# Kernel tuning notes

Hardware: AMD Instinct MI355X
Metric: run time of the kernel (lower is better)

The kernel has to match this reference:

```python
import jax, jax.numpy as jnp
import numpy as np

HEIGHT = 32
NEG = -1e30
K = 2
DEPTH_LIM = 3
BN_EPS = 1e-5


def blockwise_knn(x, k, depth_lim):
    # x: [B, C, N]. Returns global neighbor indices [B, N, k*width].
    B, C, N = x.shape
    width = N // HEIGHT
    k_eff = k * width
    xb = x.reshape(B, C, HEIGHT, width)
    win = 2 * depth_lim + 1
    offs = jnp.arange(win) - depth_lim

    def per_block(i):
        wb = i + offs
        valid = (wb >= 0) & (wb < HEIGHT)
        wbc = jnp.clip(wb, 0, HEIGHT - 1)
        cand = xb[:, :, wbc, :].reshape(B, C, win * width)   # [B,C,W]
        q = xb[:, :, i, :]                                   # [B,C,width]
        # negative squared distance: 2 q.c - |q|^2 - |c|^2 (topk largest = nearest)
        d = 2.0 * jnp.einsum('bcq,bcw->bqw', q, cand)
        d = d - jnp.sum(q * q, axis=1)[:, :, None] - jnp.sum(cand * cand, axis=1)[:, None, :]
        mask = jnp.repeat(valid, width)                      # [W]
        d = jnp.where(mask[None, None, :], d, NEG)
        _, loc = jax.lax.top_k(d, k_eff)                     # [B,width,k_eff]
        # window starts at block (i-depth_lim): local -> global point index
        return loc + (i - depth_lim) * width

    idx = jax.vmap(per_block, out_axes=1)(jnp.arange(HEIGHT))  # [B,32,width,k_eff]
    return idx.reshape(B, N, k_eff)


def get_graph_feature(x, k, depth_lim):
    B, C, N = x.shape
    idx = blockwise_knn(x, k, depth_lim)              # [B,N,K] int32
    xt = jnp.transpose(x, (0, 2, 1))                  # [B,N,C]
    feat = jax.vmap(lambda xb, ib: xb[ib])(xt, idx)   # [B,N,K,C] gather
    center = xt[:, :, None, :]
    f = jnp.concatenate([feat - center, jnp.broadcast_to(center, feat.shape)], axis=-1)
    return jnp.transpose(f, (0, 3, 1, 2))             # [B,2C,N,K]


def edge_layer(x, w, g, b, k, depth_lim):
    f = get_graph_feature(x, k, depth_lim)            # [B,2C,N,K]
    y = jnp.einsum('oc,bcnk->bonk', w, f)             # 1x1 conv, no bias
    # BatchNorm2d, train-mode batch statistics (biased variance)
    mu = jnp.mean(y, axis=(0, 2, 3), keepdims=True)
    var = jnp.mean((y - mu) ** 2, axis=(0, 2, 3), keepdims=True)
    y = (y - mu) / jnp.sqrt(var + BN_EPS) * g[None, :, None, None] + b[None, :, None, None]
    y = jnp.where(y >= 0, y, 0.2 * y)                 # LeakyReLU(0.2)
    return jnp.max(y, axis=-1)                        # max over neighbors -> [B,O,N]


def setup_inputs() -> dict:
    key = jax.random.key(0)
    ks = jax.random.split(key, 16)
    d = {}
    d['x'] = jax.random.normal(ks[0], (2, 256, 1024), jnp.float32)
    shapes = {'w0': (128, 512), 'w1': (128, 256), 'w2': (64, 256), 'w3': (64, 128)}
    for i, (name, sh) in enumerate(shapes.items()):
        d[name] = jax.random.normal(ks[1 + i], sh, jnp.float32) * (1.0 / np.sqrt(sh[1]))
        co = sh[0]
        d['g' + name[1]] = jax.random.uniform(ks[5 + i], (co,), jnp.float32, 0.5, 1.5)
        d['b' + name[1]] = jax.random.normal(ks[9 + i], (co,), jnp.float32) * 0.1
    d['w_last'] = jax.random.normal(ks[13], (384, 384), jnp.float32) * (1.0 / np.sqrt(384))
    return d


def reference(x, w0, g0, b0, w1, g1, b1, w2, g2, b2, w3, g3, b3, w_last):
    x0 = edge_layer(x, w0, g0, b0, K, DEPTH_LIM)          # [B,128,N]
    xnew = edge_layer(x0, w1, g1, b1, K, DEPTH_LIM)       # [B,128,N]
    xcon = jnp.concatenate([x0, xnew], axis=1)            # [B,256,N]
    xnew = edge_layer(xnew, w2, g2, b2, K, DEPTH_LIM)     # [B,64,N]
    xcon = jnp.concatenate([xcon, xnew], axis=1)          # [B,320,N]
    xnew = edge_layer(xnew, w3, g3, b3, K, DEPTH_LIM)     # [B,64,N]
    xcon = jnp.concatenate([xcon, xnew], axis=1)          # [B,384,N]
    return jnp.einsum('oc,bcn->bon', w_last, xcon)        # Conv1d k=1, no bias
```

## Files before the change

kernel.cpp:

```cpp
#include <hip/hip_runtime.h>
#include <math.h>

#define NPTS 1024
#define CAND 224
#define KEFF 64
#define BATCH 2
#define NEGV -1e30f

__global__ __launch_bounds__(256) void kprep(const float* __restrict__ w0, const float* __restrict__ w1,
                                             const float* __restrict__ w2, const float* __restrict__ w3,
                                             const float* __restrict__ wl, float* __restrict__ wt) {
    __shared__ float tA[32][33];
    __shared__ float tB[32][33];
    int id = blockIdx.x;
    int t = threadIdx.x;
    int row = t >> 5, col = t & 31;
    const float* W = w0; int Cin = 256, Co = 128; float* WtA = wt; float* WtB = wt + 32768;
    int tc = 0, to = 0; bool isWL = false;
    if (id < 32)      { int r = id;      tc = r >> 2; to = r & 3; }
    else if (id < 48) { W = w1; Cin = 128; Co = 128; WtA = wt + 65536;  WtB = wt + 81920;  int r = id - 32; tc = r >> 2; to = r & 3; }
    else if (id < 56) { W = w2; Cin = 128; Co = 64;  WtA = wt + 98304;  WtB = wt + 106496; int r = id - 48; tc = r >> 1; to = r & 1; }
    else if (id < 60) { W = w3; Cin = 64;  Co = 64;  WtA = wt + 114688; WtB = wt + 118784; int r = id - 56; tc = r >> 1; to = r & 1; }
    else { isWL = true; int r = id - 60; tc = r / 12; to = r % 12; }
    if (!isWL) {
#pragma unroll
        for (int r = 0; r < 4; ++r) {
            int o = to * 32 + row + r * 8;
            int c = tc * 32 + col;
            float va = W[(size_t)o * 2 * Cin + c];
            tA[row + r * 8][col] = va;
            tB[row + r * 8][col] = W[(size_t)o * 2 * Cin + Cin + c] - va;
        }
        __syncthreads();
#pragma unroll
        for (int r = 0; r < 4; ++r) {
            int c = tc * 32 + row + r * 8;
            int o = to * 32 + col;
            WtA[(size_t)c * Co + o] = tA[col][row + r * 8];
            WtB[(size_t)c * Co + o] = tB[col][row + r * 8];
        }
    } else {
        float* wlT = wt + 122880;
#pragma unroll
        for (int r = 0; r < 4; ++r) {
            int o = to * 32 + row + r * 8;
            int c = tc * 32 + col;
            tA[row + r * 8][col] = wl[(size_t)o * 384 + c];
        }
        __syncthreads();
#pragma unroll
        for (int r = 0; r < 4; ++r) {
            int c = tc * 32 + row + r * 8;
            int o = to * 32 + col;
            wlT[(size_t)c * 384 + o] = tA[col][row + r * 8];
        }
    }
}

struct GP {
    const float* xin; int bstride; int Cin; int Co; int nch; int applyBN;
    const float* WtA; const float* WtB;
    const float* partPrev; const float* gPrev; const float* bePrev;
    float* A; float* Bv; float* sq; float* Dp;
};

__global__ __launch_bounds__(256) void kgemm(GP p) {
    __shared__ float smem[7168];
    __shared__ float shsc[128];
    __shared__ float shsh[128];
    int t = threadIdx.x;
    if (p.applyBN && t < p.Cin) {
        const float* pp = p.partPrev;
        float s  = pp[t * 2]     + pp[(p.Cin + t) * 2];
        float s2 = pp[t * 2 + 1] + pp[(p.Cin + t) * 2 + 1];
        const float invc = 1.f / 131072.f;
        float mu = s * invc;
        float var = s2 * invc - mu * mu;
        float rs = rsqrtf(var + 1e-5f);
        float sc = p.gPrev[t] * rs;
        shsc[t] = sc;
        shsh[t] = p.bePrev[t] - mu * sc;
    }
    __syncthreads();
    int nABx = 16 * (p.Co >> 6) * BATCH;
    if ((int)blockIdx.x < nABx) {
        int id = blockIdx.x;
        int nt = id & 15; int rest = id >> 4;
        int nOT = p.Co >> 6;
        int ot = rest % nOT; int b = rest / nOT;
        int tn4 = (t & 15) * 4, to4 = (t >> 4) * 4;
        int n0 = nt * 64, o0 = ot * 64;
        const float* xb = p.xin + (size_t)b * p.bstride + n0;
        float* Xs = smem; float* Wta = smem + 2048; float* Wtb = smem + 4224;
        float4 a[4], bb[4], s4;
#pragma unroll
        for (int i = 0; i < 4; ++i) { a[i] = make_float4(0.f,0.f,0.f,0.f); bb[i] = make_float4(0.f,0.f,0.f,0.f); }
        s4 = make_float4(0.f,0.f,0.f,0.f);
        int cc0 = t >> 6, nn0 = t & 63;
        for (int c0 = 0; c0 < p.Cin; c0 += 32) {
            float rx[8], ra[8], rb[8];
#pragma unroll
            for (int k = 0; k < 8; ++k) {
                int cc = cc0 + k * 4;
                rx[k] = xb[(size_t)(c0 + cc) * NPTS + nn0];
                ra[k] = p.WtA[(size_t)(c0 + cc) * p.Co + o0 + nn0];
                rb[k] = p.WtB[(size_t)(c0 + cc) * p.Co + o0 + nn0];
            }
            if (p.applyBN) {
#pragma unroll
                for (int k = 0; k < 8; ++k) {
                    int cc = cc0 + k * 4;
                    float y = fmaf(rx[k], shsc[c0 + cc], shsh[c0 + cc]);
                    rx[k] = y >= 0.f ? y : 0.2f * y;
                }
            }
            __syncthreads();
#pragma unroll
            for (int k = 0; k < 8; ++k) {
                int cc = cc0 + k * 4;
                Xs[cc * 64 + nn0] = rx[k];
                Wta[cc * 68 + nn0] = ra[k];
                Wtb[cc * 68 + nn0] = rb[k];
            }
            __syncthreads();
#pragma unroll 4
            for (int cc = 0; cc < 32; ++cc) {
                float4 xv = *(const float4*)&Xs[cc * 64 + tn4];
                float4 wa = *(const float4*)&Wta[cc * 68 + to4];
                float4 wb = *(const float4*)&Wtb[cc * 68 + to4];
                s4.x = fmaf(xv.x, xv.x, s4.x);
                s4.y = fmaf(xv.y, xv.y, s4.y);
                s4.z = fmaf(xv.z, xv.z, s4.z);
                s4.w = fmaf(xv.w, xv.w, s4.w);
                float wav[4] = {wa.x, wa.y, wa.z, wa.w};
                float wbv[4] = {wb.x, wb.y, wb.z, wb.w};
#pragma unroll
                for (int i = 0; i < 4; ++i) {
                    a[i].x  = fmaf(wav[i], xv.x, a[i].x);
                    a[i].y  = fmaf(wav[i], xv.y, a[i].y);
                    a[i].z  = fmaf(wav[i], xv.z, a[i].z);
                    a[i].w  = fmaf(wav[i], xv.w, a[i].w);
                    bb[i].x = fmaf(wbv[i], xv.x, bb[i].x);
                    bb[i].y = fmaf(wbv[i], xv.y, bb[i].y);
                    bb[i].z = fmaf(wbv[i], xv.z, bb[i].z);
                    bb[i].w = fmaf(wbv[i], xv.w, bb[i].w);
                }
            }
        }
        int n = n0 + tn4;
        if (ot == 0 && to4 == 0)
            *(float4*)&p.sq[b * NPTS + n] = s4;
#pragma unroll
        for (int i = 0; i < 4; ++i) {
            int o = o0 + to4 + i;
            size_t off = ((size_t)(b * p.Co + o)) * NPTS + n;
            *(float4*)&p.A[off] = a[i];
            *(float4*)&p.Bv[off] = bb[i];
        }
    } else {
        int id2 = blockIdx.x - nABx;
        int chunk = id2 % p.nch; int rest = id2 / p.nch;
        int i = rest & 31; int b = rest >> 5;
        const float* xb = p.xin + (size_t)b * p.bstride;
        float* Xc = smem;
        int q = t >> 3;
        int wg = t & 7;
        float acc[28];
#pragma unroll
        for (int j = 0; j < 28; ++j) acc[j] = 0.f;
        for (int sub = 0; sub < 2; ++sub) {
            int c0 = chunk * 64 + sub * 32;
            if (c0 >= p.Cin) break;
            float r[28];
            int rcc[28], rw[28];
#pragma unroll
            for (int k = 0; k < 28; ++k) {
                int e = t + k * 256;
                int cc = e / CAND;
                int w  = e - cc * CAND;
                rcc[k] = cc; rw[k] = w;
                int wb = i - 3 + (w >> 5);
                wb = wb < 0 ? 0 : (wb > 31 ? 31 : wb);
                r[k] = xb[(size_t)(c0 + cc) * NPTS + wb * 32 + (w & 31)];
            }
            if (p.applyBN) {
#pragma unroll
                for (int k = 0; k < 28; ++k) {
                    float y = fmaf(r[k], shsc[c0 + rcc[k]], shsh[c0 + rcc[k]]);
                    r[k] = y >= 0.f ? y : 0.2f * y;
                }
            }
            __syncthreads();
#pragma unroll
            for (int k = 0; k < 28; ++k)
                Xc[rcc[k] * CAND + rw[k]] = r[k];
            __syncthreads();
            for (int cc = 0; cc < 32; ++cc) {
                float qv = Xc[cc * CAND + 96 + q];
                const float4* row = (const float4*)&Xc[cc * CAND + wg * 28];
#pragma unroll
                for (int j4 = 0; j4 < 7; ++j4) {
                    float4 v = row[j4];
                    acc[j4 * 4 + 0] = fmaf(qv, v.x, acc[j4 * 4 + 0]);
                    acc[j4 * 4 + 1] = fmaf(qv, v.y, acc[j4 * 4 + 1]);
                    acc[j4 * 4 + 2] = fmaf(qv, v.z, acc[j4 * 4 + 2]);
                    acc[j4 * 4 + 3] = fmaf(qv, v.w, acc[j4 * 4 + 3]);
                }
            }
        }
        int n = i * 32 + q;
        size_t base = (((size_t)chunk * BATCH + b) * NPTS + n) * CAND + wg * 28;
        float4* outp = (float4*)&p.Dp[base];
#pragma unroll
        for (int j4 = 0; j4 < 7; ++j4)
            outp[j4] = make_float4(acc[j4 * 4], acc[j4 * 4 + 1], acc[j4 * 4 + 2], acc[j4 * 4 + 3]);
    }
}

template<int NCH>
__global__ __launch_bounds__(256) void kselect(const float* __restrict__ Dp,
                                               const float* __restrict__ sq,
                                               int* __restrict__ idxo) {
    __shared__ ulonglong2 Dsh2[4][112];
    unsigned long long* Dsh = (unsigned long long*)Dsh2;
    int t = threadIdx.x;
    int wv = t >> 6, l = t & 63;
    int b = blockIdx.y;
    int n = blockIdx.x * 4 + wv;
    int i = n >> 5;
    float sqn = sq[b * NPTS + n];
    float pr[4][NCH];
    float sqw[4];
#pragma unroll
    for (int j = 0; j < 4; ++j) {
        int w = l + 64 * j;
        if (w < CAND) {
            size_t off = ((size_t)b * NPTS + n) * CAND + w;
#pragma unroll
            for (int ch = 0; ch < NCH; ++ch)
                pr[j][ch] = Dp[off + (size_t)ch * (BATCH * NPTS * CAND)];
            int wb = i - 3 + (w >> 5);
            int wbc = wb < 0 ? 0 : (wb > 31 ? 31 : wb);
            sqw[j] = sq[b * NPTS + wbc * 32 + (w & 31)];
        }
    }
    unsigned long long kj[4];
#pragma unroll
    for (int j = 0; j < 4; ++j) {
        int w = l + 64 * j;
        if (w < CAND) {
            float s = 0.f;
#pragma unroll
            for (int ch = 0; ch < NCH; ++ch) s += pr[j][ch];
            int wb = i - 3 + (w >> 5);
            bool valid = (wb >= 0) && (wb < 32);
            float d = 2.f * s - sqn - sqw[j];
            d = valid ? d : NEGV;
            unsigned u = __float_as_uint(d);
            u ^= ((unsigned)((int)u >> 31)) | 0x80000000u;
            unsigned long long key = ((unsigned long long)u << 8) | (unsigned long long)(255 - w);
            kj[j] = key;
            Dsh[wv * 224 + w] = key;
        } else {
            kj[j] = 0ull;
        }
    }
    __syncthreads();
    int cnt[4] = {0, 0, 0, 0};
    const ulonglong2* row = Dsh2[wv];
#pragma unroll 2
    for (int w2 = 0; w2 < 112; w2 += 4) {
        ulonglong2 k0 = row[w2], k1 = row[w2 + 1], k2 = row[w2 + 2], k3 = row[w2 + 3];
#pragma unroll
        for (int j = 0; j < 4; ++j) {
            unsigned long long kk = kj[j];
            cnt[j] += (int)(k0.x > kk) + (int)(k0.y > kk) + (int)(k1.x > kk) + (int)(k1.y > kk)
                    + (int)(k2.x > kk) + (int)(k2.y > kk) + (int)(k3.x > kk) + (int)(k3.y > kk);
        }
    }
#pragma unroll
    for (int j = 0; j < 4; ++j) {
        int w = l + 64 * j;
        if (w < CAND && cnt[j] < KEFF)
            idxo[((size_t)b * NPTS + n) * KEFF + cnt[j]] = (i - 3) * 32 + w;
    }
}

__global__ __launch_bounds__(256) void kagg(const float* __restrict__ A, const float* __restrict__ Bv,
                                            const int* __restrict__ idx, int Co,
                                            float* __restrict__ xconM, int chOut,
                                            float* __restrict__ part) {
    __shared__ float Ash[NPTS];
    __shared__ float red[256];
    int o = blockIdx.x, b = blockIdx.y, t = threadIdx.x;
    size_t rowoff = ((size_t)(b * Co + o)) * NPTS;
    {
        float rA[4];
#pragma unroll
        for (int r = 0; r < 4; ++r) rA[r] = A[rowoff + r * 256 + t];
#pragma unroll
        for (int r = 0; r < 4; ++r) Ash[r * 256 + t] = rA[r];
    }
    __syncthreads();
    float sum = 0.f, sumsq = 0.f;
    for (int r = 0; r < 4; ++r) {
        int n = r * 256 + t;
        const int4* ip = (const int4*)&idx[((size_t)b * NPTS + n) * KEFF];
        float s1 = 0.f, s2 = 0.f, mx = -3.4e38f;
#pragma unroll
        for (int kk = 0; kk < KEFF / 4; ++kk) {
            int4 v4 = ip[kk];
            float a0 = Ash[v4.x], a1 = Ash[v4.y], a2 = Ash[v4.z], a3 = Ash[v4.w];
            s1 += a0 + a1 + a2 + a3;
            s2 += a0 * a0 + a1 * a1 + a2 * a2 + a3 * a3;
            mx = fmaxf(mx, fmaxf(fmaxf(a0, a1), fmaxf(a2, a3)));
        }
        float bv = Bv[rowoff + n];
        xconM[((size_t)b * 384 + chOut + o) * NPTS + n] = mx + bv;
        sum   += s1 + 64.f * bv;
        sumsq += s2 + 2.f * bv * s1 + 64.f * bv * bv;
    }
    red[t] = sum; __syncthreads();
    for (int s = 128; s > 0; s >>= 1) { if (t < s) red[t] += red[t + s]; __syncthreads(); }
    if (t == 0) part[((size_t)(b * Co + o)) * 2 + 0] = red[0];
    __syncthreads();
    red[t] = sumsq; __syncthreads();
    for (int s = 128; s > 0; s >>= 1) { if (t < s) red[t] += red[t + s]; __syncthreads(); }
    if (t == 0) part[((size_t)(b * Co + o)) * 2 + 1] = red[0];
}

struct FP {
    const float* part0; const float* part1; const float* part2; const float* part3;
    const float* g0; const float* g1; const float* g2; const float* g3;
    const float* be0; const float* be1; const float* be2; const float* be3;
};

__global__ __launch_bounds__(256) void kfinal(const float* __restrict__ xconM,
                                              const float* __restrict__ wlT, FP p,
                                              float* __restrict__ out) {
    __shared__ float Xs[2048];
    __shared__ float Wl[2176];
    __shared__ float shsc[384];
    __shared__ float shsh[384];
    int t = threadIdx.x;
    for (int ch = t; ch < 384; ch += 256) {
        const float* pl; const float* gl; const float* bl; int o, Col;
        if (ch < 128)      { pl = p.part0; gl = p.g0; bl = p.be0; o = ch;       Col = 128; }
        else if (ch < 256) { pl = p.part1; gl = p.g1; bl = p.be1; o = ch - 128; Col = 128; }
        else if (ch < 320) { pl = p.part2; gl = p.g2; bl = p.be2; o = ch - 256; Col = 64;  }
        else               { pl = p.part3; gl = p.g3; bl = p.be3; o = ch - 320; Col = 64;  }
        float s  = pl[o * 2]     + pl[(Col + o) * 2];
        float s2 = pl[o * 2 + 1] + pl[(Col + o) * 2 + 1];
        const float invc = 1.f / 131072.f;
        float mu = s * invc;
        float var = s2 * invc - mu * mu;
        float rs = rsqrtf(var + 1e-5f);
        float sc = gl[o] * rs;
        shsc[ch] = sc;
        shsh[ch] = bl[o] - mu * sc;
    }
    __syncthreads();
    int tn4 = (t & 15) * 4, to4 = (t >> 4) * 4;
    int n0 = blockIdx.x * 64, o0 = blockIdx.y * 64, b = blockIdx.z;
    int cc0 = t >> 6, nn0 = t & 63;
    float4 acc[4];
#pragma unroll
    for (int i = 0; i < 4; ++i) acc[i] = make_float4(0.f,0.f,0.f,0.f);
    for (int c0 = 0; c0 < 384; c0 += 32) {
        float rx[8], rw[8];
#pragma unroll
        for (int k = 0; k < 8; ++k) {
            int cc = cc0 + k * 4;
            rx[k] = xconM[((size_t)b * 384 + c0 + cc) * NPTS + n0 + nn0];
            rw[k] = wlT[(size_t)(c0 + cc) * 384 + o0 + nn0];
        }
#pragma unroll
        for (int k = 0; k < 8; ++k) {
            int cc = cc0 + k * 4;
            float y = fmaf(rx[k], shsc[c0 + cc], shsh[c0 + cc]);
            rx[k] = y >= 0.f ? y : 0.2f * y;
        }
        __syncthreads();
#pragma unroll
        for (int k = 0; k < 8; ++k) {
            int cc = cc0 + k * 4;
            Xs[cc * 64 + nn0] = rx[k];
            Wl[cc * 68 + nn0] = rw[k];
        }
        __syncthreads();
#pragma unroll 4
        for (int cc = 0; cc < 32; ++cc) {
            float4 xv = *(const float4*)&Xs[cc * 64 + tn4];
            float4 wv = *(const float4*)&Wl[cc * 68 + to4];
            float wvv[4] = {wv.x, wv.y, wv.z, wv.w};
#pragma unroll
            for (int i = 0; i < 4; ++i) {
                acc[i].x = fmaf(wvv[i], xv.x, acc[i].x);
                acc[i].y = fmaf(wvv[i], xv.y, acc[i].y);
                acc[i].z = fmaf(wvv[i], xv.z, acc[i].z);
                acc[i].w = fmaf(wvv[i], xv.w, acc[i].w);
            }
        }
    }
#pragma unroll
    for (int i = 0; i < 4; ++i)
        *(float4*)&out[((size_t)b * 384 + o0 + to4 + i) * NPTS + n0 + tn4] = acc[i];
}

extern "C" void kernel_launch(void* const* d_in, const int* in_sizes, int n_in,
                              void* d_out, int out_size, void* d_ws, size_t ws_size,
                              hipStream_t stream) {
    const float* x  = (const float*)d_in[0];
    const float* w[4]  = {(const float*)d_in[1], (const float*)d_in[4], (const float*)d_in[7], (const float*)d_in[10]};
    const float* g[4]  = {(const float*)d_in[2], (const float*)d_in[5], (const float*)d_in[8], (const float*)d_in[11]};
    const float* be[4] = {(const float*)d_in[3], (const float*)d_in[6], (const float*)d_in[9], (const float*)d_in[12]};
    const float* wl = (const float*)d_in[13];

    float* ws    = (float*)d_ws;
    float* xconM = ws;
    float* A     = xconM + 786432;
    float* Bv    = A + 262144;
    float* sq    = Bv + 262144;
    float* Dp    = sq + 2048;
    float* part  = Dp + 1835008;
    float* wt    = part + 2048;
    int*   idx   = (int*)(wt + 270336);

    kprep<<<204, 256, 0, stream>>>(w[0], w[1], w[2], w[3], wl, wt);

    struct LC { const float* xin; int bstride; int Cin; int Co; int nch; int chOut;
                const float* wtA; const float* wtB; };
    LC L[4] = {
        { x,                  256 * 1024, 256, 128, 4, 0,   wt,          wt + 32768  },
        { xconM,              384 * 1024, 128, 128, 2, 128, wt + 65536,  wt + 81920  },
        { xconM + 128 * 1024, 384 * 1024, 128, 64,  2, 256, wt + 98304,  wt + 106496 },
        { xconM + 256 * 1024, 384 * 1024, 64,  64,  1, 320, wt + 114688, wt + 118784 },
    };

    for (int l = 0; l < 4; ++l) {
        GP gp;
        gp.xin = L[l].xin; gp.bstride = L[l].bstride; gp.Cin = L[l].Cin; gp.Co = L[l].Co;
        gp.nch = L[l].nch; gp.applyBN = (l > 0);
        gp.WtA = L[l].wtA; gp.WtB = L[l].wtB;
        gp.partPrev = (l > 0) ? part + (l - 1) * 512 : nullptr;
        gp.gPrev = (l > 0) ? g[l - 1] : nullptr;
        gp.bePrev = (l > 0) ? be[l - 1] : nullptr;
        gp.A = A; gp.Bv = Bv; gp.sq = sq; gp.Dp = Dp;
        int nAB = 16 * (L[l].Co >> 6) * BATCH;
        int nDist = L[l].nch * 32 * BATCH;
        kgemm  <<<nAB + nDist, 256, 0, stream>>>(gp);
        if (L[l].nch == 4)      kselect<4><<<dim3(NPTS / 4, BATCH), 256, 0, stream>>>(Dp, sq, idx);
        else if (L[l].nch == 2) kselect<2><<<dim3(NPTS / 4, BATCH), 256, 0, stream>>>(Dp, sq, idx);
        else                    kselect<1><<<dim3(NPTS / 4, BATCH), 256, 0, stream>>>(Dp, sq, idx);
        kagg   <<<dim3(L[l].Co, BATCH), 256, 0, stream>>>(A, Bv, idx, L[l].Co, xconM, L[l].chOut, part + l * 512);
    }

    FP fp;
    fp.part0 = part; fp.part1 = part + 512; fp.part2 = part + 1024; fp.part3 = part + 1536;
    fp.g0 = g[0]; fp.g1 = g[1]; fp.g2 = g[2]; fp.g3 = g[3];
    fp.be0 = be[0]; fp.be1 = be[1]; fp.be2 = be[2]; fp.be3 = be[3];
    kfinal<<<dim3(16, 6, BATCH), 256, 0, stream>>>(xconM, wt + 122880, fp, (float*)d_out);
}
```

Measured before the change: 277.1 us.

## Fuse distance computation and top-k selection into the GEMM kernel

Merges the kselect kernel into the distance blocks of the GEMM kernel. Each block now loops over all channel chunks itself, computes the squared norms of the candidate window locally, and ranks the 224 candidate keys in shared memory. This removes the Dp partial-distance buffer, the global sq array and one launch per layer. In exchange only 64 distance blocks run per layer, down from up to 256 chunk-split blocks, and each thread holds 28 keys and 28 counters, which raises register pressure and lowers parallelism.

New measurement: 411.8 us. 1.49x slower.

```diff
diff --git a/kernel.cpp b/kernel.cpp
--- a/kernel.cpp
+++ b/kernel.cpp
@@ -58,16 +58,18 @@
 }
 
 struct GP {
-    const float* xin; int bstride; int Cin; int Co; int nch; int applyBN;
+    const float* xin; int bstride; int Cin; int Co; int applyBN;
     const float* WtA; const float* WtB;
     const float* partPrev; const float* gPrev; const float* bePrev;
-    float* A; float* Bv; float* sq; float* Dp;
+    float* A; float* Bv; int* idxo;
 };
 
-__global__ __launch_bounds__(256) void kgemm(GP p) {
-    __shared__ float smem[7168];
+__global__ __launch_bounds__(256) void kfused(GP p) {
+    __shared__ __align__(16) unsigned long long sKeys[32 * 224];
+    __shared__ float sqc[224];
     __shared__ float shsc[128];
     __shared__ float shsh[128];
+    float* smem = (float*)sKeys;
     int t = threadIdx.x;
     if (p.applyBN && t < p.Cin) {
         const float* pp = p.partPrev;
@@ -92,10 +94,9 @@
         int n0 = nt * 64, o0 = ot * 64;
         const float* xb = p.xin + (size_t)b * p.bstride + n0;
         float* Xs = smem; float* Wta = smem + 2048; float* Wtb = smem + 4224;
-        float4 a[4], bb[4], s4;
+        float4 a[4], bb[4];
 #pragma unroll
         for (int i = 0; i < 4; ++i) { a[i] = make_float4(0.f,0.f,0.f,0.f); bb[i] = make_float4(0.f,0.f,0.f,0.f); }
-        s4 = make_float4(0.f,0.f,0.f,0.f);
         int cc0 = t >> 6, nn0 = t & 63;
         for (int c0 = 0; c0 < p.Cin; c0 += 32) {
             float rx[8], ra[8], rb[8];
@@ -128,10 +129,6 @@
                 float4 xv = *(const float4*)&Xs[cc * 64 + tn4];
                 float4 wa = *(const float4*)&Wta[cc * 68 + to4];
                 float4 wb = *(const float4*)&Wtb[cc * 68 + to4];
-                s4.x = fmaf(xv.x, xv.x, s4.x);
-                s4.y = fmaf(xv.y, xv.y, s4.y);
-                s4.z = fmaf(xv.z, xv.z, s4.z);
-                s4.w = fmaf(xv.w, xv.w, s4.w);
                 float wav[4] = {wa.x, wa.y, wa.z, wa.w};
                 float wbv[4] = {wb.x, wb.y, wb.z, wb.w};
 #pragma unroll
@@ -148,8 +145,6 @@
             }
         }
         int n = n0 + tn4;
-        if (ot == 0 && to4 == 0)
-            *(float4*)&p.sq[b * NPTS + n] = s4;
 #pragma unroll
         for (int i = 0; i < 4; ++i) {
             int o = o0 + to4 + i;
@@ -159,130 +154,109 @@
         }
     } else {
         int id2 = blockIdx.x - nABx;
-        int chunk = id2 % p.nch; int rest = id2 / p.nch;
-        int i = rest & 31; int b = rest >> 5;
+        int i = id2 & 31, b = id2 >> 5;
         const float* xb = p.xin + (size_t)b * p.bstride;
         float* Xc = smem;
         int q = t >> 3;
         int wg = t & 7;
-        float acc[28];
-#pragma unroll
-        for (int j = 0; j < 28; ++j) acc[j] = 0.f;
-        for (int sub = 0; sub < 2; ++sub) {
-            int c0 = chunk * 64 + sub * 32;
-            if (c0 >= p.Cin) break;
-            float r[28];
-            int rcc[28], rw[28];
-#pragma unroll
-            for (int k = 0; k < 28; ++k) {
-                int e = t + k * 256;
-                int cc = e / CAND;
-                int w  = e - cc * CAND;
-                rcc[k] = cc; rw[k] = w;
-                int wb = i - 3 + (w >> 5);
-                wb = wb < 0 ? 0 : (wb > 31 ? 31 : wb);
-                r[k] = xb[(size_t)(c0 + cc) * NPTS + wb * 32 + (w & 31)];
-            }
-            if (p.applyBN) {
+        float s28[28];
+#pragma unroll
+        for (int j = 0; j < 28; ++j) s28[j] = 0.f;
+        float sqacc = 0.f;
+        int nch = (p.Cin + 63) >> 6;
+        for (int chunk = 0; chunk < nch; ++chunk) {
+            float cacc[28];
+#pragma unroll
+            for (int j = 0; j < 28; ++j) cacc[j] = 0.f;
+            for (int sub = 0; sub < 2; ++sub) {
+                int c0 = chunk * 64 + sub * 32;
+                if (c0 >= p.Cin) break;
+                float r[28];
+                int rcc[28], rw[28];
 #pragma unroll
                 for (int k = 0; k < 28; ++k) {
-                    float y = fmaf(r[k], shsc[c0 + rcc[k]], shsh[c0 + rcc[k]]);
-                    r[k] = y >= 0.f ? y : 0.2f * y;
-                }
-            }
-            __syncthreads();
-#pragma unroll
-            for (int k = 0; k < 28; ++k)
-                Xc[rcc[k] * CAND + rw[k]] = r[k];
-            __syncthreads();
-            for (int cc = 0; cc < 32; ++cc) {
-                float qv = Xc[cc * CAND + 96 + q];
-                const float4* row = (const float4*)&Xc[cc * CAND + wg * 28];
-#pragma unroll
-                for (int j4 = 0; j4 < 7; ++j4) {
-                    float4 v = row[j4];
-                    acc[j4 * 4 + 0] = fmaf(qv, v.x, acc[j4 * 4 + 0]);
-                    acc[j4 * 4 + 1] = fmaf(qv, v.y, acc[j4 * 4 + 1]);
-                    acc[j4 * 4 + 2] = fmaf(qv, v.z, acc[j4 * 4 + 2]);
-                    acc[j4 * 4 + 3] = fmaf(qv, v.w, acc[j4 * 4 + 3]);
-                }
-            }
-        }
-        int n = i * 32 + q;
-        size_t base = (((size_t)chunk * BATCH + b) * NPTS + n) * CAND + wg * 28;
-        float4* outp = (float4*)&p.Dp[base];
-#pragma unroll
-        for (int j4 = 0; j4 < 7; ++j4)
-            outp[j4] = make_float4(acc[j4 * 4], acc[j4 * 4 + 1], acc[j4 * 4 + 2], acc[j4 * 4 + 3]);
-    }
-}
-
-template<int NCH>
-__global__ __launch_bounds__(256) void kselect(const float* __restrict__ Dp,
-                                               const float* __restrict__ sq,
-                                               int* __restrict__ idxo) {
-    __shared__ ulonglong2 Dsh2[4][112];
-    unsigned long long* Dsh = (unsigned long long*)Dsh2;
-    int t = threadIdx.x;
-    int wv = t >> 6, l = t & 63;
-    int b = blockIdx.y;
-    int n = blockIdx.x * 4 + wv;
-    int i = n >> 5;
-    float sqn = sq[b * NPTS + n];
-    float pr[4][NCH];
-    float sqw[4];
-#pragma unroll
-    for (int j = 0; j < 4; ++j) {
-        int w = l + 64 * j;
-        if (w < CAND) {
-            size_t off = ((size_t)b * NPTS + n) * CAND + w;
-#pragma unroll
-            for (int ch = 0; ch < NCH; ++ch)
-                pr[j][ch] = Dp[off + (size_t)ch * (BATCH * NPTS * CAND)];
-            int wb = i - 3 + (w >> 5);
-            int wbc = wb < 0 ? 0 : (wb > 31 ? 31 : wb);
-            sqw[j] = sq[b * NPTS + wbc * 32 + (w & 31)];
-        }
-    }
-    unsigned long long kj[4];
-#pragma unroll
-    for (int j = 0; j < 4; ++j) {
-        int w = l + 64 * j;
-        if (w < CAND) {
-            float s = 0.f;
-#pragma unroll
-            for (int ch = 0; ch < NCH; ++ch) s += pr[j][ch];
+                    int e = t + k * 256;
+                    int cc = e / CAND;
+                    int w  = e - cc * CAND;
+                    rcc[k] = cc; rw[k] = w;
+                    int wb = i - 3 + (w >> 5);
+                    wb = wb < 0 ? 0 : (wb > 31 ? 31 : wb);
+                    r[k] = xb[(size_t)(c0 + cc) * NPTS + wb * 32 + (w & 31)];
+                }
+                if (p.applyBN) {
+#pragma unroll
+                    for (int k = 0; k < 28; ++k) {
+                        float y = fmaf(r[k], shsc[c0 + rcc[k]], shsh[c0 + rcc[k]]);
+                        r[k] = y >= 0.f ? y : 0.2f * y;
+                    }
+                }
+                __syncthreads();
+#pragma unroll
+                for (int k = 0; k < 28; ++k)
+                    Xc[rcc[k] * CAND + rw[k]] = r[k];
+                __syncthreads();
+                if (t < CAND) {
+#pragma unroll 8
+                    for (int cc = 0; cc < 32; ++cc) {
+                        float v = Xc[cc * CAND + t];
+                        sqacc = fmaf(v, v, sqacc);
+                    }
+                }
+                for (int cc = 0; cc < 32; ++cc) {
+                    float qv = Xc[cc * CAND + 96 + q];
+                    const float4* row = (const float4*)&Xc[cc * CAND + wg * 28];
+#pragma unroll
+                    for (int j4 = 0; j4 < 7; ++j4) {
+                        float4 v = row[j4];
+                        cacc[j4 * 4 + 0] = fmaf(qv, v.x, cacc[j4 * 4 + 0]);
+                        cacc[j4 * 4 + 1] = fmaf(qv, v.y, cacc[j4 * 4 + 1]);
+                        cacc[j4 * 4 + 2] = fmaf(qv, v.z, cacc[j4 * 4 + 2]);
+                        cacc[j4 * 4 + 3] = fmaf(qv, v.w, cacc[j4 * 4 + 3]);
+                    }
+                }
+            }
+#pragma unroll
+            for (int j = 0; j < 28; ++j) s28[j] += cacc[j];
+        }
+        if (t < CAND) sqc[t] = sqacc;
+        __syncthreads();
+        float sqn = sqc[96 + q];
+        unsigned long long kj[28];
+#pragma unroll
+        for (int j = 0; j < 28; ++j) {
+            int w = wg * 28 + j;
             int wb = i - 3 + (w >> 5);
             bool valid = (wb >= 0) && (wb < 32);
-            float d = 2.f * s - sqn - sqw[j];
+            float d = 2.f * s28[j] - sqn - sqc[w];
             d = valid ? d : NEGV;
             unsigned u = __float_as_uint(d);
             u ^= ((unsigned)((int)u >> 31)) | 0x80000000u;
-            unsigned long long key = ((unsigned long long)u << 8) | (unsigned long long)(255 - w);
-            kj[j] = key;
-            Dsh[wv * 224 + w] = key;
-        } else {
-            kj[j] = 0ull;
-        }
-    }
-    __syncthreads();
-    int cnt[4] = {0, 0, 0, 0};
-    const ulonglong2* row = Dsh2[wv];
-#pragma unroll 2
-    for (int w2 = 0; w2 < 112; w2 += 4) {
-        ulonglong2 k0 = row[w2], k1 = row[w2 + 1], k2 = row[w2 + 2], k3 = row[w2 + 3];
-#pragma unroll
-        for (int j = 0; j < 4; ++j) {
-            unsigned long long kk = kj[j];
-            cnt[j] += (int)(k0.x > kk) + (int)(k0.y > kk) + (int)(k1.x > kk) + (int)(k1.y > kk)
-                    + (int)(k2.x > kk) + (int)(k2.y > kk) + (int)(k3.x > kk) + (int)(k3.y > kk);
-        }
-    }
-#pragma unroll
-    for (int j = 0; j < 4; ++j) {
-        int w = l + 64 * j;
-        if (w < CAND && cnt[j] < KEFF)
-            idxo[((size_t)b * NPTS + n) * KEFF + cnt[j]] = (i - 3) * 32 + w;
+            kj[j] = ((unsigned long long)u << 8) | (unsigned long long)(255 - w);
+        }
+#pragma unroll
+        for (int j = 0; j < 28; ++j)
+            sKeys[q * 224 + wg * 28 + j] = kj[j];
+        __syncthreads();
+        int cnt[28];
+#pragma unroll
+        for (int j = 0; j < 28; ++j) cnt[j] = 0;
+        const ulonglong2* row = (const ulonglong2*)(sKeys + q * 224);
+        for (int c2 = 0; c2 < 112; c2 += 4) {
+            ulonglong2 k0 = row[c2], k1 = row[c2 + 1], k2 = row[c2 + 2], k3 = row[c2 + 3];
+#pragma unroll
+            for (int j = 0; j < 28; ++j) {
+                unsigned long long kk = kj[j];
+                cnt[j] += (int)(k0.x > kk) + (int)(k0.y > kk) + (int)(k1.x > kk) + (int)(k1.y > kk)
+                        + (int)(k2.x > kk) + (int)(k2.y > kk) + (int)(k3.x > kk) + (int)(k3.y > kk);
+            }
+        }
+        int n = i * 32 + q;
+#pragma unroll
+        for (int j = 0; j < 28; ++j) {
+            int w = wg * 28 + j;
+            if (cnt[j] < KEFF)
+                p.idxo[((size_t)b * NPTS + n) * KEFF + cnt[j]] = (i - 3) * 32 + w;
+        }
     }
 }
 
@@ -420,39 +394,33 @@
     float* xconM = ws;
     float* A     = xconM + 786432;
     float* Bv    = A + 262144;
-    float* sq    = Bv + 262144;
-    float* Dp    = sq + 2048;
-    float* part  = Dp + 1835008;
+    float* part  = Bv + 262144;
     float* wt    = part + 2048;
     int*   idx   = (int*)(wt + 270336);
 
     kprep<<<204, 256, 0, stream>>>(w[0], w[1], w[2], w[3], wl, wt);
 
-    struct LC { const float* xin; int bstride; int Cin; int Co; int nch; int chOut;
+    struct LC { const float* xin; int bstride; int Cin; int Co; int chOut;
                 const float* wtA; const float* wtB; };
     LC L[4] = {
-        { x,                  256 * 1024, 256, 128, 4, 0,   wt,          wt + 32768  },
-        { xconM,              384 * 1024, 128, 128, 2, 128, wt + 65536,  wt + 81920  },
-        { xconM + 128 * 1024, 384 * 1024, 128, 64,  2, 256, wt + 98304,  wt + 106496 },
-        { xconM + 256 * 1024, 384 * 1024, 64,  64,  1, 320, wt + 114688, wt + 118784 },
+        { x,                  256 * 1024, 256, 128, 0,   wt,          wt + 32768  },
+        { xconM,              384 * 1024, 128, 128, 128, wt + 65536,  wt + 81920  },
+        { xconM + 128 * 1024, 384 * 1024, 128, 64,  256, wt + 98304,  wt + 106496 },
+        { xconM + 256 * 1024, 384 * 1024, 64,  64,  320, wt + 114688, wt + 118784 },
     };
 
     for (int l = 0; l < 4; ++l) {
         GP gp;
         gp.xin = L[l].xin; gp.bstride = L[l].bstride; gp.Cin = L[l].Cin; gp.Co = L[l].Co;
-        gp.nch = L[l].nch; gp.applyBN = (l > 0);
+        gp.applyBN = (l > 0);
         gp.WtA = L[l].wtA; gp.WtB = L[l].wtB;
         gp.partPrev = (l > 0) ? part + (l - 1) * 512 : nullptr;
         gp.gPrev = (l > 0) ? g[l - 1] : nullptr;
         gp.bePrev = (l > 0) ? be[l - 1] : nullptr;
-        gp.A = A; gp.Bv = Bv; gp.sq = sq; gp.Dp = Dp;
+        gp.A = A; gp.Bv = Bv; gp.idxo = idx;
         int nAB = 16 * (L[l].Co >> 6) * BATCH;
-        int nDist = L[l].nch * 32 * BATCH;
-        kgemm  <<<nAB + nDist, 256, 0, stream>>>(gp);
-        if (L[l].nch == 4)      kselect<4><<<dim3(NPTS / 4, BATCH), 256, 0, stream>>>(Dp, sq, idx);
-        else if (L[l].nch == 2) kselect<2><<<dim3(NPTS / 4, BATCH), 256, 0, stream>>>(Dp, sq, idx);
-        else                    kselect<1><<<dim3(NPTS / 4, BATCH), 256, 0, stream>>>(Dp, sq, idx);
-        kagg   <<<dim3(L[l].Co, BATCH), 256, 0, stream>>>(A, Bv, idx, L[l].Co, xconM, L[l].chOut, part + l * 512);
+        kfused<<<nAB + 64, 256, 0, stream>>>(gp);
+        kagg  <<<dim3(L[l].Co, BATCH), 256, 0, stream>>>(A, Bv, idx, L[l].Co, xconM, L[l].chOut, part + l * 512);
     }
 
     FP fp;
```

## Split GEMM and distance work into more blocks, transpose neighbor index layout

Applied to the files above, without the earlier changes.

The A/B projection GEMM tiles shrink from 64 to 32 points, doubling the block count. The distance blocks now each handle a single 32-channel slice, which doubles the number of channel chunks and the partial-distance buffer that kselect must sum. The neighbor index array is stored k-major, so kagg threads read the indices for consecutive points with coalesced loads. The aim is more parallelism on a small problem, paid for with extra partial-sum memory traffic in kselect and a larger workspace.

Result: faster. 258.7 us, median of 2 (-6.7%).

```diff
diff --git a/kernel.cpp b/kernel.cpp
--- a/kernel.cpp
+++ b/kernel.cpp
@@ -6,6 +6,7 @@
 #define KEFF 64
 #define BATCH 2
 #define NEGV -1e30f
+#define PLANE (BATCH * NPTS * CAND)
 
 __global__ __launch_bounds__(256) void kprep(const float* __restrict__ w0, const float* __restrict__ w1,
                                              const float* __restrict__ w2, const float* __restrict__ w3,
@@ -82,130 +83,123 @@
         shsh[t] = p.bePrev[t] - mu * sc;
     }
     __syncthreads();
-    int nABx = 16 * (p.Co >> 6) * BATCH;
+    int nOT = p.Co >> 6;
+    int nABx = 32 * nOT * BATCH;
     if ((int)blockIdx.x < nABx) {
         int id = blockIdx.x;
-        int nt = id & 15; int rest = id >> 4;
-        int nOT = p.Co >> 6;
+        int nt = id & 31; int rest = id >> 5;
         int ot = rest % nOT; int b = rest / nOT;
-        int tn4 = (t & 15) * 4, to4 = (t >> 4) * 4;
-        int n0 = nt * 64, o0 = ot * 64;
+        int tn2 = (t & 15) * 2, to4 = (t >> 4) * 4;
+        int n0 = nt * 32, o0 = ot * 64;
         const float* xb = p.xin + (size_t)b * p.bstride + n0;
-        float* Xs = smem; float* Wta = smem + 2048; float* Wtb = smem + 4224;
-        float4 a[4], bb[4], s4;
-#pragma unroll
-        for (int i = 0; i < 4; ++i) { a[i] = make_float4(0.f,0.f,0.f,0.f); bb[i] = make_float4(0.f,0.f,0.f,0.f); }
-        s4 = make_float4(0.f,0.f,0.f,0.f);
-        int cc0 = t >> 6, nn0 = t & 63;
+        float* Xs = smem; float* Wta = smem + 1024; float* Wtb = smem + 3200;
+        float2 a2[4], b2[4], s2v;
+#pragma unroll
+        for (int i = 0; i < 4; ++i) { a2[i] = make_float2(0.f,0.f); b2[i] = make_float2(0.f,0.f); }
+        s2v = make_float2(0.f,0.f);
+        int xcc0 = t >> 5, xnn = t & 31;
+        int wcc0 = t >> 6, woo = t & 63;
         for (int c0 = 0; c0 < p.Cin; c0 += 32) {
-            float rx[8], ra[8], rb[8];
+            float rx[4], ra[8], rb[8];
+#pragma unroll
+            for (int k = 0; k < 4; ++k)
+                rx[k] = xb[(size_t)(c0 + xcc0 + k * 8) * NPTS + xnn];
 #pragma unroll
             for (int k = 0; k < 8; ++k) {
-                int cc = cc0 + k * 4;
-                rx[k] = xb[(size_t)(c0 + cc) * NPTS + nn0];
-                ra[k] = p.WtA[(size_t)(c0 + cc) * p.Co + o0 + nn0];
-                rb[k] = p.WtB[(size_t)(c0 + cc) * p.Co + o0 + nn0];
+                ra[k] = p.WtA[(size_t)(c0 + wcc0 + k * 4) * p.Co + o0 + woo];
+                rb[k] = p.WtB[(size_t)(c0 + wcc0 + k * 4) * p.Co + o0 + woo];
             }
             if (p.applyBN) {
 #pragma unroll
-                for (int k = 0; k < 8; ++k) {
-                    int cc = cc0 + k * 4;
+                for (int k = 0; k < 4; ++k) {
+                    int cc = xcc0 + k * 8;
                     float y = fmaf(rx[k], shsc[c0 + cc], shsh[c0 + cc]);
                     rx[k] = y >= 0.f ? y : 0.2f * y;
                 }
             }
             __syncthreads();
 #pragma unroll
+            for (int k = 0; k < 4; ++k)
+                Xs[(xcc0 + k * 8) * 32 + xnn] = rx[k];
+#pragma unroll
             for (int k = 0; k < 8; ++k) {
-                int cc = cc0 + k * 4;
-                Xs[cc * 64 + nn0] = rx[k];
-                Wta[cc * 68 + nn0] = ra[k];
-                Wtb[cc * 68 + nn0] = rb[k];
+                Wta[(wcc0 + k * 4) * 68 + woo] = ra[k];
+                Wtb[(wcc0 + k * 4) * 68 + woo] = rb[k];
             }
             __syncthreads();
-#pragma unroll 4
+#pragma unroll 8
             for (int cc = 0; cc < 32; ++cc) {
-                float4 xv = *(const float4*)&Xs[cc * 64 + tn4];
+                float2 xv = *(const float2*)&Xs[cc * 32 + tn2];
                 float4 wa = *(const float4*)&Wta[cc * 68 + to4];
                 float4 wb = *(const float4*)&Wtb[cc * 68 + to4];
-                s4.x = fmaf(xv.x, xv.x, s4.x);
-                s4.y = fmaf(xv.y, xv.y, s4.y);
-                s4.z = fmaf(xv.z, xv.z, s4.z);
-                s4.w = fmaf(xv.w, xv.w, s4.w);
+                s2v.x = fmaf(xv.x, xv.x, s2v.x);
+                s2v.y = fmaf(xv.y, xv.y, s2v.y);
                 float wav[4] = {wa.x, wa.y, wa.z, wa.w};
                 float wbv[4] = {wb.x, wb.y, wb.z, wb.w};
 #pragma unroll
                 for (int i = 0; i < 4; ++i) {
-                    a[i].x  = fmaf(wav[i], xv.x, a[i].x);
-                    a[i].y  = fmaf(wav[i], xv.y, a[i].y);
-                    a[i].z  = fmaf(wav[i], xv.z, a[i].z);
-                    a[i].w  = fmaf(wav[i], xv.w, a[i].w);
-                    bb[i].x = fmaf(wbv[i], xv.x, bb[i].x);
-                    bb[i].y = fmaf(wbv[i], xv.y, bb[i].y);
-                    bb[i].z = fmaf(wbv[i], xv.z, bb[i].z);
-                    bb[i].w = fmaf(wbv[i], xv.w, bb[i].w);
+                    a2[i].x = fmaf(wav[i], xv.x, a2[i].x);
+                    a2[i].y = fmaf(wav[i], xv.y, a2[i].y);
+                    b2[i].x = fmaf(wbv[i], xv.x, b2[i].x);
+                    b2[i].y = fmaf(wbv[i], xv.y, b2[i].y);
                 }
             }
         }
-        int n = n0 + tn4;
+        int n = n0 + tn2;
         if (ot == 0 && to4 == 0)
-            *(float4*)&p.sq[b * NPTS + n] = s4;
+            *(float2*)&p.sq[b * NPTS + n] = s2v;
 #pragma unroll
         for (int i = 0; i < 4; ++i) {
             int o = o0 + to4 + i;
             size_t off = ((size_t)(b * p.Co + o)) * NPTS + n;
-            *(float4*)&p.A[off] = a[i];
-            *(float4*)&p.Bv[off] = bb[i];
+            *(float2*)&p.A[off] = a2[i];
+            *(float2*)&p.Bv[off] = b2[i];
         }
     } else {
         int id2 = blockIdx.x - nABx;
         int chunk = id2 % p.nch; int rest = id2 / p.nch;
         int i = rest & 31; int b = rest >> 5;
+        int c0 = chunk * 32;
         const float* xb = p.xin + (size_t)b * p.bstride;
         float* Xc = smem;
         int q = t >> 3;
         int wg = t & 7;
+        float r[28];
+        int rcc[28], rw[28];
+#pragma unroll
+        for (int k = 0; k < 28; ++k) {
+            int e = t + k * 256;
+            int cc = e / CAND;
+            int w  = e - cc * CAND;
+            rcc[k] = cc; rw[k] = w;
+            int wb = i - 3 + (w >> 5);
+            wb = wb < 0 ? 0 : (wb > 31 ? 31 : wb);
+            r[k] = xb[(size_t)(c0 + cc) * NPTS + wb * 32 + (w & 31)];
+        }
+        if (p.applyBN) {
+#pragma unroll
+            for (int k = 0; k < 28; ++k) {
+                float y = fmaf(r[k], shsc[c0 + rcc[k]], shsh[c0 + rcc[k]]);
+                r[k] = y >= 0.f ? y : 0.2f * y;
+            }
+        }
+#pragma unroll
+        for (int k = 0; k < 28; ++k)
+            Xc[rcc[k] * CAND + rw[k]] = r[k];
+        __syncthreads();
         float acc[28];
 #pragma unroll
         for (int j = 0; j < 28; ++j) acc[j] = 0.f;
-        for (int sub = 0; sub < 2; ++sub) {
-            int c0 = chunk * 64 + sub * 32;
-            if (c0 >= p.Cin) break;
-            float r[28];
-            int rcc[28], rw[28];
-#pragma unroll
-            for (int k = 0; k < 28; ++k) {
-                int e = t + k * 256;
-                int cc = e / CAND;
-                int w  = e - cc * CAND;
-                rcc[k] = cc; rw[k] = w;
-                int wb = i - 3 + (w >> 5);
-                wb = wb < 0 ? 0 : (wb > 31 ? 31 : wb);
-                r[k] = xb[(size_t)(c0 + cc) * NPTS + wb * 32 + (w & 31)];
-            }
-            if (p.applyBN) {
-#pragma unroll
-                for (int k = 0; k < 28; ++k) {
-                    float y = fmaf(r[k], shsc[c0 + rcc[k]], shsh[c0 + rcc[k]]);
-                    r[k] = y >= 0.f ? y : 0.2f * y;
-                }
-            }
-            __syncthreads();
-#pragma unroll
-            for (int k = 0; k < 28; ++k)
-                Xc[rcc[k] * CAND + rw[k]] = r[k];
-            __syncthreads();
-            for (int cc = 0; cc < 32; ++cc) {
-                float qv = Xc[cc * CAND + 96 + q];
-                const float4* row = (const float4*)&Xc[cc * CAND + wg * 28];
-#pragma unroll
-                for (int j4 = 0; j4 < 7; ++j4) {
-                    float4 v = row[j4];
-                    acc[j4 * 4 + 0] = fmaf(qv, v.x, acc[j4 * 4 + 0]);
-                    acc[j4 * 4 + 1] = fmaf(qv, v.y, acc[j4 * 4 + 1]);
-                    acc[j4 * 4 + 2] = fmaf(qv, v.z, acc[j4 * 4 + 2]);
-                    acc[j4 * 4 + 3] = fmaf(qv, v.w, acc[j4 * 4 + 3]);
-                }
+        for (int cc = 0; cc < 32; ++cc) {
+            float qv = Xc[cc * CAND + 96 + q];
+            const float4* row = (const float4*)&Xc[cc * CAND + wg * 28];
+#pragma unroll
+            for (int j4 = 0; j4 < 7; ++j4) {
+                float4 v = row[j4];
+                acc[j4 * 4 + 0] = fmaf(qv, v.x, acc[j4 * 4 + 0]);
+                acc[j4 * 4 + 1] = fmaf(qv, v.y, acc[j4 * 4 + 1]);
+                acc[j4 * 4 + 2] = fmaf(qv, v.z, acc[j4 * 4 + 2]);
+                acc[j4 * 4 + 3] = fmaf(qv, v.w, acc[j4 * 4 + 3]);
             }
         }
         int n = i * 32 + q;
@@ -238,7 +232,7 @@
             size_t off = ((size_t)b * NPTS + n) * CAND + w;
 #pragma unroll
             for (int ch = 0; ch < NCH; ++ch)
-                pr[j][ch] = Dp[off + (size_t)ch * (BATCH * NPTS * CAND)];
+                pr[j][ch] = Dp[off + (size_t)ch * PLANE];
             int wb = i - 3 + (w >> 5);
             int wbc = wb < 0 ? 0 : (wb > 31 ? 31 : wb);
             sqw[j] = sq[b * NPTS + wbc * 32 + (w & 31)];
@@ -282,7 +276,7 @@
     for (int j = 0; j < 4; ++j) {
         int w = l + 64 * j;
         if (w < CAND && cnt[j] < KEFF)
-            idxo[((size_t)b * NPTS + n) * KEFF + cnt[j]] = (i - 3) * 32 + w;
+            idxo[((size_t)b * KEFF + cnt[j]) * NPTS + n] = (i - 3) * 32 + w;
     }
 }
 
@@ -305,15 +299,23 @@
     float sum = 0.f, sumsq = 0.f;
     for (int r = 0; r < 4; ++r) {
         int n = r * 256 + t;
-        const int4* ip = (const int4*)&idx[((size_t)b * NPTS + n) * KEFF];
+        const int* ip = idx + (size_t)b * KEFF * NPTS + n;
         float s1 = 0.f, s2 = 0.f, mx = -3.4e38f;
 #pragma unroll
-        for (int kk = 0; kk < KEFF / 4; ++kk) {
-            int4 v4 = ip[kk];
-            float a0 = Ash[v4.x], a1 = Ash[v4.y], a2 = Ash[v4.z], a3 = Ash[v4.w];
-            s1 += a0 + a1 + a2 + a3;
-            s2 += a0 * a0 + a1 * a1 + a2 * a2 + a3 * a3;
-            mx = fmaxf(mx, fmaxf(fmaxf(a0, a1), fmaxf(a2, a3)));
+        for (int kb = 0; kb < 4; ++kb) {
+            int iv[16];
+#pragma unroll
+            for (int m = 0; m < 16; ++m)
+                iv[m] = ip[(size_t)(kb * 16 + m) * NPTS];
+            float av[16];
+#pragma unroll
+            for (int m = 0; m < 16; ++m) av[m] = Ash[iv[m]];
+#pragma unroll
+            for (int m = 0; m < 16; m += 4) {
+                s1 += av[m] + av[m+1] + av[m+2] + av[m+3];
+                s2 += av[m]*av[m] + av[m+1]*av[m+1] + av[m+2]*av[m+2] + av[m+3]*av[m+3];
+                mx = fmaxf(mx, fmaxf(fmaxf(av[m], av[m+1]), fmaxf(av[m+2], av[m+3])));
+            }
         }
         float bv = Bv[rowoff + n];
         xconM[((size_t)b * 384 + chOut + o) * NPTS + n] = mx + bv;
@@ -422,7 +424,7 @@
     float* Bv    = A + 262144;
     float* sq    = Bv + 262144;
     float* Dp    = sq + 2048;
-    float* part  = Dp + 1835008;
+    float* part  = Dp + 3670016;
     float* wt    = part + 2048;
     int*   idx   = (int*)(wt + 270336);
 
@@ -431,10 +433,10 @@
     struct LC { const float* xin; int bstride; int Cin; int Co; int nch; int chOut;
                 const float* wtA; const float* wtB; };
     LC L[4] = {
-        { x,                  256 * 1024, 256, 128, 4, 0,   wt,          wt + 32768  },
-        { xconM,              384 * 1024, 128, 128, 2, 128, wt + 65536,  wt + 81920  },
-        { xconM + 128 * 1024, 384 * 1024, 128, 64,  2, 256, wt + 98304,  wt + 106496 },
-        { xconM + 256 * 1024, 384 * 1024, 64,  64,  1, 320, wt + 114688, wt + 118784 },
+        { x,                  256 * 1024, 256, 128, 8, 0,   wt,          wt + 32768  },
+        { xconM,              384 * 1024, 128, 128, 4, 128, wt + 65536,  wt + 81920  },
+        { xconM + 128 * 1024, 384 * 1024, 128, 64,  4, 256, wt + 98304,  wt + 106496 },
+        { xconM + 256 * 1024, 384 * 1024, 64,  64,  2, 320, wt + 114688, wt + 118784 },
     };
 
     for (int l = 0; l < 4; ++l) {
@@ -446,13 +448,13 @@
         gp.gPrev = (l > 0) ? g[l - 1] : nullptr;
         gp.bePrev = (l > 0) ? be[l - 1] : nullptr;
         gp.A = A; gp.Bv = Bv; gp.sq = sq; gp.Dp = Dp;
-        int nAB = 16 * (L[l].Co >> 6) * BATCH;
+        int nAB = 32 * (L[l].Co >> 6) * BATCH;
         int nDist = L[l].nch * 32 * BATCH;
-        kgemm  <<<nAB + nDist, 256, 0, stream>>>(gp);
-        if (L[l].nch == 4)      kselect<4><<<dim3(NPTS / 4, BATCH), 256, 0, stream>>>(Dp, sq, idx);
-        else if (L[l].nch == 2) kselect<2><<<dim3(NPTS / 4, BATCH), 256, 0, stream>>>(Dp, sq, idx);
-        else                    kselect<1><<<dim3(NPTS / 4, BATCH), 256, 0, stream>>>(Dp, sq, idx);
-        kagg   <<<dim3(L[l].Co, BATCH), 256, 0, stream>>>(A, Bv, idx, L[l].Co, xconM, L[l].chOut, part + l * 512);
+        kgemm<<<nAB + nDist, 256, 0, stream>>>(gp);
+        if (L[l].nch == 8)      kselect<8><<<dim3(NPTS / 4, BATCH), 256, 0, stream>>>(Dp, sq, idx);
+        else if (L[l].nch == 4) kselect<4><<<dim3(NPTS / 4, BATCH), 256, 0, stream>>>(Dp, sq, idx);
+        else                    kselect<2><<<dim3(NPTS / 4, BATCH), 256, 0, stream>>>(Dp, sq, idx);
+        kagg<<<dim3(L[l].Co, BATCH), 256, 0, stream>>>(A, Bv, idx, L[l].Co, xconM, L[l].chOut, part + l * 512);
     }
 
     FP fp;
```
